# Performance work log

Measured on AMD Instinct MI355X. Metric: run time of the kernel, lower is better.

Reference implementation:

```python
import jax, jax.numpy as jnp
import numpy as np

HIDDEN = 512
BATCH = 64
SEQ = 1024
FUTURE = 16


def setup_inputs() -> dict:
    key = jax.random.key(0)
    ks = jax.random.split(key, 12)
    s = 0.05  # small init to keep the un-squashed LSTM recurrence stable
    H = HIDDEN
    inp = {
        "x": jax.random.normal(ks[0], (BATCH, SEQ), dtype=jnp.float32),
        # cell 1: input_length=1
        "W1": jax.random.normal(ks[1], (4 * H, 1), dtype=jnp.float32) * s,
        "bW1": jax.random.normal(ks[2], (4 * H,), dtype=jnp.float32) * s,
        "U1": jax.random.normal(ks[3], (4 * H, H), dtype=jnp.float32) * s,
        "bU1": jax.random.normal(ks[4], (4 * H,), dtype=jnp.float32) * s,
        # cell 2: input_length=H
        "W2": jax.random.normal(ks[5], (4 * H, H), dtype=jnp.float32) * s,
        "bW2": jax.random.normal(ks[6], (4 * H,), dtype=jnp.float32) * s,
        "U2": jax.random.normal(ks[7], (4 * H, H), dtype=jnp.float32) * s,
        "bU2": jax.random.normal(ks[8], (4 * H,), dtype=jnp.float32) * s,
        # output head: Linear(H, 1)
        "lw": jax.random.normal(ks[9], (1, H), dtype=jnp.float32) * s,
        "lb": jax.random.normal(ks[10], (1,), dtype=jnp.float32) * s,
        "future": FUTURE,
    }
    return inp


def _cell(x_t, h, c, W, bW, U, bU):
    # NOTE: faithful to source — NO sigmoid/tanh on the gates, only tanh on c_t.
    gates = x_t @ W.T + bW + h @ U.T + bU            # [B, 4H]
    i_t, f_t, g_t, o_t = jnp.split(gates, 4, axis=-1)
    c_t = f_t * c + i_t * g_t
    h_t = o_t * jnp.tanh(c_t)
    return h_t, c_t


def reference(x, W1, bW1, U1, bU1, W2, bW2, U2, bU2, lw, lb, future):
    B = x.shape[0]
    H = U1.shape[1]
    zeros = jnp.zeros((B, H), dtype=x.dtype)
    init = (zeros, zeros, zeros, zeros, jnp.zeros((B, 1), dtype=x.dtype))

    def run(carry, x_t):
        h1, c1, h2, c2, _ = carry
        h1, c1 = _cell(x_t, h1, c1, W1, bW1, U1, bU1)
        h2, c2 = _cell(h1, h2, c2, W2, bW2, U2, bU2)
        out = h2 @ lw.T + lb                          # [B, 1]
        return (h1, c1, h2, c2, out), out

    # teacher-forced pass over the observed sequence
    xs = x.T[:, :, None]                              # [T, B, 1]
    carry, outs = jax.lax.scan(run, init, xs)         # outs: [T, B, 1]

    if future > 0:
        def run_future(carry, _):
            return run(carry, carry[4])
        carry, outs_f = jax.lax.scan(run_future, carry, None, length=future)
        outs = jnp.concatenate([outs, outs_f], axis=0)

    return outs[:, :, 0].T                            # [B, T+future]
```

## Files before the change

kernel.cpp:

```cpp
#include <hip/hip_runtime.h>
#include <math.h>

#define HID 512
#define B 64
#define SEQT 1024
#define FUT 16
#define TT (SEQT + FUT)
#define NWG 256
#define TPB 512
#define TPB1 1024
#define NWAVE1 16
#define JPW 2
#define HB (HID * B)
#define BLOBF 12288

#define WS_H1_F   512
#define WS_H2_F   (WS_H1_F + 2 * HB)
#define WS_BLOB_F (WS_H2_F + 2 * HB)
#define WS_XT_F   (WS_BLOB_F + NWG * BLOBF)
#define WS_TOT_F  (WS_XT_F + SEQT * B)

__device__ inline void pub_store(float* p, float v) {
  __hip_atomic_store(p, v, __ATOMIC_RELAXED, __HIP_MEMORY_SCOPE_AGENT);
}

__device__ inline void gbar4(int* bb, int wg, int bar) {
  __builtin_amdgcn_s_waitcnt(0);
  __syncthreads();
  const int tid  = threadIdx.x;
  const int lane = tid & 63;
  if (tid == 0) {
    __hip_atomic_store(bb + wg, bar, __ATOMIC_RELAXED, __HIP_MEMORY_SCOPE_AGENT);
    __builtin_amdgcn_fence(__ATOMIC_ACQUIRE, "agent");
  }
  if (wg == NWG - 1 && tid < 64) {
    for (;;) {
      int a = __hip_atomic_load(bb + lane,       __ATOMIC_RELAXED, __HIP_MEMORY_SCOPE_AGENT);
      int b = __hip_atomic_load(bb + 64  + lane, __ATOMIC_RELAXED, __HIP_MEMORY_SCOPE_AGENT);
      int c = __hip_atomic_load(bb + 128 + lane, __ATOMIC_RELAXED, __HIP_MEMORY_SCOPE_AGENT);
      int d = __hip_atomic_load(bb + 192 + lane, __ATOMIC_RELAXED, __HIP_MEMORY_SCOPE_AGENT);
      if (__all(a >= bar && b >= bar && c >= bar && d >= bar)) break;
      __builtin_amdgcn_s_sleep(2);
    }
    if (lane == 0)
      __hip_atomic_store(bb + 320, bar, __ATOMIC_RELAXED, __HIP_MEMORY_SCOPE_AGENT);
  }
  if (tid == 0) {
    while (__hip_atomic_load(bb + 320, __ATOMIC_RELAXED,
                             __HIP_MEMORY_SCOPE_AGENT) < bar) {
      __builtin_amdgcn_s_sleep(2);
    }
  }
  __syncthreads();
}

__global__ void __launch_bounds__(256) prep_ws(
    const float* __restrict__ x,
    const float* __restrict__ U1, const float* __restrict__ W2,
    const float* __restrict__ U2, float* __restrict__ ws)
{
  const int idx = blockIdx.x * blockDim.x + threadIdx.x;
  if (idx < WS_BLOB_F) {
    ws[idx] = 0.0f;
  }
  {
    const int i2 = idx - WS_BLOB_F;
    if (i2 >= 0 && i2 < NWG * BLOBF) {
      const int wg  = i2 / BLOBF;
      const int off = i2 - wg * BLOBF;
      const int j0  = wg * JPW;
      float v;
      if (off < 4096) {
        const int k = off >> 3, r = off & 7;
        const int row = (r >> 1) * HID + j0 + (r & 1);
        v = U1[(size_t)row * HID + k];
      } else {
        const int o2 = off - 4096;
        const int k = o2 >> 4, rr = o2 & 15;
        const int r = rr & 7;
        const int row = (r >> 1) * HID + j0 + (r & 1);
        v = (rr < 8) ? W2[(size_t)row * HID + k] : U2[(size_t)row * HID + k];
      }
      ws[WS_BLOB_F + i2] = v;
    }
  }
  {
    const int i3 = idx - WS_XT_F;
    if (i3 >= 0 && i3 < SEQT * B) {
      const int t = i3 >> 6, b = i3 & 63;
      ws[WS_XT_F + i3] = x[(size_t)b * SEQT + t];
    }
  }
}

__global__ void __launch_bounds__(TPB1, 1) rnn_main(
    const float* __restrict__ W1, const float* __restrict__ bW1,
    const float* __restrict__ bU1,
    const float* __restrict__ bW2, const float* __restrict__ bU2,
    const float* __restrict__ lw, const float* __restrict__ lb,
    float* __restrict__ out,
    int* __restrict__ bb,
    float* __restrict__ h1b, float* __restrict__ h2b,
    const float* __restrict__ wbl, const float* __restrict__ xT)
{
  __shared__ float wlds[BLOBF];
  __shared__ float red[NWAVE1][8][B];
  __shared__ float outred[NWAVE1][B];
  __shared__ float c1s[JPW][B], c2s[JPW][B];
  __shared__ float w1c[8], bs1[8], bs2[8];

  const int wg   = blockIdx.x;
  const int j0   = wg * JPW;
  const int tid  = threadIdx.x;
  const int lane = tid & 63;
  const int wvu  = __builtin_amdgcn_readfirstlane(tid >> 6);

  {
    const float4* gsrc = (const float4*)(wbl + (size_t)wg * BLOBF);
    float4* ldst = (float4*)wlds;
    #pragma unroll
    for (int i = 0; i < BLOBF / 4 / TPB1; ++i)
      ldst[i * TPB1 + tid] = gsrc[i * TPB1 + tid];
  }
  if (tid < JPW * B) { c1s[tid >> 6][lane] = 0.f; c2s[tid >> 6][lane] = 0.f; }
  if (tid < 8) {
    const int g = tid >> 1, jl = tid & 1;
    const int row = g * HID + j0 + jl;
    w1c[tid] = W1[row];
    bs1[tid] = bW1[row] + bU1[row];
    bs2[tid] = bW2[row] + bU2[row];
  }
  __syncthreads();

  const float* wl1 = wlds + wvu * 256;
  const float* wl2 = wlds + 4096 + wvu * 512;
  const float lbv = lb[0];

  float4 H1[8], Q[8];
  #pragma unroll
  for (int i = 0; i < 8; ++i) H1[i] = make_float4(0.f, 0.f, 0.f, 0.f);

  int bar = 0;
  for (int t = 0; t < TT; ++t) {
    float*       h1new = h1b + (t & 1) * HB;
    const float* h2old = h2b + ((t + 1) & 1) * HB;
    float*       h2new = h2b + (t & 1) * HB;

    float xvpref = 0.f;
    if (tid < JPW * B && t < SEQT) xvpref = xT[(size_t)t * B + lane];

    {
      float a[8] = {0.f,0.f,0.f,0.f,0.f,0.f,0.f,0.f};
      #pragma unroll
      for (int c = 0; c < 8; ++c) {
        const float hh[4] = {H1[c].x, H1[c].y, H1[c].z, H1[c].w};
        #pragma unroll
        for (int j = 0; j < 4; ++j) {
          const float4 wA = *(const float4*)(wl1 + c * 32 + j * 8);
          const float4 wB = *(const float4*)(wl1 + c * 32 + j * 8 + 4);
          const float h = hh[j];
          a[0] = fmaf(wA.x, h, a[0]); a[1] = fmaf(wA.y, h, a[1]);
          a[2] = fmaf(wA.z, h, a[2]); a[3] = fmaf(wA.w, h, a[3]);
          a[4] = fmaf(wB.x, h, a[4]); a[5] = fmaf(wB.y, h, a[5]);
          a[6] = fmaf(wB.z, h, a[6]); a[7] = fmaf(wB.w, h, a[7]);
        }
      }
      #pragma unroll
      for (int r = 0; r < 8; ++r) red[wvu][r][lane] = a[r];
    }
    __syncthreads();

    if (tid < JPW * B) {
      const int jl = tid >> 6, b = tid & 63;
      const float xv = (t < SEQT) ? xvpref : out[(size_t)b * TT + (t - 1)];
      float gate[4];
      #pragma unroll
      for (int g = 0; g < 4; ++g) {
        const int r = g * 2 + jl;
        float s = bs1[r] + xv * w1c[r];
        #pragma unroll
        for (int w = 0; w < NWAVE1; ++w) s += red[w][r][b];
        gate[g] = s;
      }
      const float c = gate[1] * c1s[jl][b] + gate[0] * gate[2];
      c1s[jl][b] = c;
      const int j = j0 + jl;
      pub_store(&h1new[(size_t)(j >> 2) * (B * 4) + b * 4 + (j & 3)],
                gate[3] * tanhf(c));
    }

    ++bar;
    gbar4(bb, wg, bar);

    if (wg == (t & 127) && t >= 1 && t <= SEQT - 1) {
      const float4* hb2 = (const float4*)h2old + (size_t)(wvu * 8) * B + lane;
      const float4* lw4 = (const float4*)lw + wvu * 8;
      float p = 0.f;
      #pragma unroll
      for (int i = 0; i < 8; ++i) {
        const float4 hv = hb2[i * B];
        const float4 wv = lw4[i];
        p = fmaf(wv.x, hv.x, p); p = fmaf(wv.y, hv.y, p);
        p = fmaf(wv.z, hv.z, p); p = fmaf(wv.w, hv.w, p);
      }
      outred[wvu][lane] = p;
      __syncthreads();
      if (tid < B) {
        float o = lbv;
        #pragma unroll
        for (int s = 0; s < NWAVE1; ++s) o += outred[s][tid];
        pub_store(&out[(size_t)tid * TT + (t - 1)], o);
      }
      __syncthreads();
    }

    {
      const float4* pp4 = (const float4*)h1new + (size_t)(wvu * 8) * B + lane;
      const float4* qq4 = (const float4*)h2old + (size_t)(wvu * 8) * B + lane;
      #pragma unroll
      for (int i = 0; i < 8; ++i) H1[i] = pp4[i * B];
      #pragma unroll
      for (int i = 0; i < 8; ++i) Q[i] = qq4[i * B];
      float a[8] = {0.f,0.f,0.f,0.f,0.f,0.f,0.f,0.f};
      #pragma unroll
      for (int c = 0; c < 8; ++c) {
        const float hp_[4] = {H1[c].x, H1[c].y, H1[c].z, H1[c].w};
        const float hq_[4] = {Q[c].x, Q[c].y, Q[c].z, Q[c].w};
        #pragma unroll
        for (int j = 0; j < 4; ++j) {
          const float4 w0 = *(const float4*)(wl2 + c * 64 + j * 16);
          const float4 w1 = *(const float4*)(wl2 + c * 64 + j * 16 + 4);
          const float4 w2 = *(const float4*)(wl2 + c * 64 + j * 16 + 8);
          const float4 w3 = *(const float4*)(wl2 + c * 64 + j * 16 + 12);
          const float hp1 = hp_[j], hq1 = hq_[j];
          a[0] = fmaf(w0.x, hp1, a[0]); a[1] = fmaf(w0.y, hp1, a[1]);
          a[2] = fmaf(w0.z, hp1, a[2]); a[3] = fmaf(w0.w, hp1, a[3]);
          a[4] = fmaf(w1.x, hp1, a[4]); a[5] = fmaf(w1.y, hp1, a[5]);
          a[6] = fmaf(w1.z, hp1, a[6]); a[7] = fmaf(w1.w, hp1, a[7]);
          a[0] = fmaf(w2.x, hq1, a[0]); a[1] = fmaf(w2.y, hq1, a[1]);
          a[2] = fmaf(w2.z, hq1, a[2]); a[3] = fmaf(w2.w, hq1, a[3]);
          a[4] = fmaf(w3.x, hq1, a[4]); a[5] = fmaf(w3.y, hq1, a[5]);
          a[6] = fmaf(w3.z, hq1, a[6]); a[7] = fmaf(w3.w, hq1, a[7]);
        }
      }
      #pragma unroll
      for (int r = 0; r < 8; ++r) red[wvu][r][lane] = a[r];
    }
    __syncthreads();

    if (tid < JPW * B) {
      const int jl = tid >> 6, b = tid & 63;
      float gate[4];
      #pragma unroll
      for (int g = 0; g < 4; ++g) {
        const int r = g * 2 + jl;
        float s = bs2[r];
        #pragma unroll
        for (int w = 0; w < NWAVE1; ++w) s += red[w][r][b];
        gate[g] = s;
      }
      const float c = gate[1] * c2s[jl][b] + gate[0] * gate[2];
      c2s[jl][b] = c;
      const int j = j0 + jl;
      pub_store(&h2new[(size_t)(j >> 2) * (B * 4) + b * 4 + (j & 3)],
                gate[3] * tanhf(c));
    }
    __syncthreads();

    if (t >= SEQT - 1) {
      ++bar;
      gbar4(bb, wg, bar);
      if (wg == 0) {
        const float4* hb2 = (const float4*)h2new + (size_t)(wvu * 8) * B + lane;
        const float4* lw4 = (const float4*)lw + wvu * 8;
        float p = 0.f;
        #pragma unroll
        for (int i = 0; i < 8; ++i) {
          const float4 hv = hb2[i * B];
          const float4 wv = lw4[i];
          p = fmaf(wv.x, hv.x, p); p = fmaf(wv.y, hv.y, p);
          p = fmaf(wv.z, hv.z, p); p = fmaf(wv.w, hv.w, p);
        }
        outred[wvu][lane] = p;
        __syncthreads();
        if (tid < B) {
          float o = lbv;
          #pragma unroll
          for (int s = 0; s < NWAVE1; ++s) o += outred[s][tid];
          pub_store(&out[(size_t)tid * TT + t], o);
        }
        __syncthreads();
      }
      ++bar;
      gbar4(bb, wg, bar);
    }
  }
}

__device__ inline void gbar(int* cnt, int target) {
  __syncthreads();
  if (threadIdx.x == 0) {
    __threadfence();
    __hip_atomic_fetch_add(cnt, 1, __ATOMIC_RELEASE, __HIP_MEMORY_SCOPE_AGENT);
    while (__hip_atomic_load(cnt, __ATOMIC_ACQUIRE, __HIP_MEMORY_SCOPE_AGENT) < target) {
      __builtin_amdgcn_s_sleep(2);
    }
  }
  __syncthreads();
}

__global__ void __launch_bounds__(TPB) zero_ws(float* ws, int n) {
  int i = blockIdx.x * blockDim.x + threadIdx.x;
  if (i < n) ws[i] = 0.0f;
}

__global__ void __launch_bounds__(TPB) rnn_fallback(
    const float* __restrict__ x,
    const float* __restrict__ W1, const float* __restrict__ bW1,
    const float* __restrict__ U1, const float* __restrict__ bU1,
    const float* __restrict__ W2, const float* __restrict__ bW2,
    const float* __restrict__ U2, const float* __restrict__ bU2,
    const float* __restrict__ lw, const float* __restrict__ lb,
    float* out, float* ws)
{
  __shared__ float red[8][8][B];
  __shared__ float outred[8][B];
  __shared__ float c1s[JPW][B], c2s[JPW][B];
  __shared__ float w1c[8], bs1[8], bs2[8];

  int* cnt   = (int*)ws;
  float* h1b = ws + 16;
  float* h2b = h1b + 2 * HB;

  const int wg   = blockIdx.x;
  const int j0   = wg * JPW;
  const int tid  = threadIdx.x;
  const int lane = tid & 63;
  const int wvu  = __builtin_amdgcn_readfirstlane(tid >> 6);
  const int kb   = wvu << 6;

  if (tid < JPW * B) { c1s[tid >> 6][lane] = 0.f; c2s[tid >> 6][lane] = 0.f; }
  if (tid < 8) {
    const int g = tid >> 1, jl = tid & 1;
    const int row = g * HID + j0 + jl;
    w1c[tid] = W1[row];
    bs1[tid] = bW1[row] + bU1[row];
    bs2[tid] = bW2[row] + bU2[row];
  }
  __syncthreads();

  const float* u1p[8]; const float* w2p[8]; const float* u2p[8];
  #pragma unroll
  for (int r = 0; r < 8; ++r) {
    const int row = (r >> 1) * HID + j0 + (r & 1);
    u1p[r] = U1 + (size_t)row * HID + kb;
    w2p[r] = W2 + (size_t)row * HID + kb;
    u2p[r] = U2 + (size_t)row * HID + kb;
  }
  const float lbv = lb[0];

  int bar = 0;
  for (int t = 0; t < TT; ++t) {
    const float* h1old = h1b + ((t + 1) & 1) * HB;
    float*       h1new = h1b + (t & 1) * HB;
    const float* h2old = h2b + ((t + 1) & 1) * HB;
    float*       h2new = h2b + (t & 1) * HB;

    {
      const float* hp = h1old + (size_t)kb * B;
      float a0=0.f,a1=0.f,a2=0.f,a3=0.f,a4=0.f,a5=0.f,a6=0.f,a7=0.f;
      #pragma unroll 8
      for (int k = 0; k < 64; ++k) {
        const float hv = hp[k * B + lane];
        a0 = fmaf(u1p[0][k], hv, a0); a1 = fmaf(u1p[1][k], hv, a1);
        a2 = fmaf(u1p[2][k], hv, a2); a3 = fmaf(u1p[3][k], hv, a3);
        a4 = fmaf(u1p[4][k], hv, a4); a5 = fmaf(u1p[5][k], hv, a5);
        a6 = fmaf(u1p[6][k], hv, a6); a7 = fmaf(u1p[7][k], hv, a7);
      }
      red[wvu][0][lane]=a0; red[wvu][1][lane]=a1; red[wvu][2][lane]=a2; red[wvu][3][lane]=a3;
      red[wvu][4][lane]=a4; red[wvu][5][lane]=a5; red[wvu][6][lane]=a6; red[wvu][7][lane]=a7;
    }
    __syncthreads();

    if (tid < JPW * B) {
      const int jl = tid >> 6, b = tid & 63;
      const float xv = (t < SEQT) ? x[(size_t)b * SEQT + t]
                                  : out[(size_t)b * TT + (t - 1)];
      float gate[4];
      #pragma unroll
      for (int g = 0; g < 4; ++g) {
        const int r = g * 2 + jl;
        float s = bs1[r] + xv * w1c[r];
        #pragma unroll
        for (int w = 0; w < 8; ++w) s += red[w][r][b];
        gate[g] = s;
      }
      const float c = gate[1] * c1s[jl][b] + gate[0] * gate[2];
      c1s[jl][b] = c;
      h1new[(size_t)(j0 + jl) * B + b] = gate[3] * tanhf(c);
    }

    ++bar;
    gbar(cnt, NWG * bar);

    if (wg == 0 && t >= 1 && t <= SEQT - 1) {
      const float* hb2 = h2old + (size_t)(wvu * 64) * B;
      const float* lwp = lw + wvu * 64;
      float p = 0.f;
      #pragma unroll 8
      for (int j = 0; j < 64; ++j) p = fmaf(lwp[j], hb2[j * B + lane], p);
      outred[wvu][lane] = p;
      __syncthreads();
      if (tid < B) {
        float o = lbv;
        #pragma unroll
        for (int s = 0; s < 8; ++s) o += outred[s][tid];
        out[(size_t)tid * TT + (t - 1)] = o;
      }
      __syncthreads();
    }

    {
      const float* h1p = h1new + (size_t)kb * B;
      const float* h2p = h2old + (size_t)kb * B;
      float s0=0.f,s1=0.f,s2=0.f,s3=0.f,s4=0.f,s5=0.f,s6=0.f,s7=0.f;
      float q0=0.f,q1=0.f,q2=0.f,q3=0.f,q4=0.f,q5=0.f,q6=0.f,q7=0.f;
      #pragma unroll 4
      for (int k = 0; k < 64; ++k) {
        const float h1v = h1p[k * B + lane];
        const float h2v = h2p[k * B + lane];
        s0 = fmaf(w2p[0][k], h1v, s0); q0 = fmaf(u2p[0][k], h2v, q0);
        s1 = fmaf(w2p[1][k], h1v, s1); q1 = fmaf(u2p[1][k], h2v, q1);
        s2 = fmaf(w2p[2][k], h1v, s2); q2 = fmaf(u2p[2][k], h2v, q2);
        s3 = fmaf(w2p[3][k], h1v, s3); q3 = fmaf(u2p[3][k], h2v, q3);
        s4 = fmaf(w2p[4][k], h1v, s4); q4 = fmaf(u2p[4][k], h2v, q4);
        s5 = fmaf(w2p[5][k], h1v, s5); q5 = fmaf(u2p[5][k], h2v, q5);
        s6 = fmaf(w2p[6][k], h1v, s6); q6 = fmaf(u2p[6][k], h2v, q6);
        s7 = fmaf(w2p[7][k], h1v, s7); q7 = fmaf(u2p[7][k], h2v, q7);
      }
      red[wvu][0][lane]=s0+q0; red[wvu][1][lane]=s1+q1;
      red[wvu][2][lane]=s2+q2; red[wvu][3][lane]=s3+q3;
      red[wvu][4][lane]=s4+q4; red[wvu][5][lane]=s5+q5;
      red[wvu][6][lane]=s6+q6; red[wvu][7][lane]=s7+q7;
    }
    __syncthreads();

    if (tid < JPW * B) {
      const int jl = tid >> 6, b = tid & 63;
      float gate[4];
      #pragma unroll
      for (int g = 0; g < 4; ++g) {
        const int r = g * 2 + jl;
        float s = bs2[r];
        #pragma unroll
        for (int w = 0; w < 8; ++w) s += red[w][r][b];
        gate[g] = s;
      }
      const float c = gate[1] * c2s[jl][b] + gate[0] * gate[2];
      c2s[jl][b] = c;
      h2new[(size_t)(j0 + jl) * B + b] = gate[3] * tanhf(c);
    }
    __syncthreads();

    if (t >= SEQT - 1) {
      ++bar;
      gbar(cnt, NWG * bar);
      if (wg == 0) {
        const float* hb2 = h2new + (size_t)(wvu * 64) * B;
        const float* lwp = lw + wvu * 64;
        float p = 0.f;
        #pragma unroll 8
        for (int j = 0; j < 64; ++j) p = fmaf(lwp[j], hb2[j * B + lane], p);
        outred[wvu][lane] = p;
        __syncthreads();
        if (tid < B) {
          float o = lbv;
          #pragma unroll
          for (int s = 0; s < 8; ++s) o += outred[s][tid];
          out[(size_t)tid * TT + t] = o;
        }
        __syncthreads();
      }
      ++bar;
      gbar(cnt, NWG * bar);
    }
  }
}

extern "C" void kernel_launch(void* const* d_in, const int* in_sizes, int n_in,
                              void* d_out, int out_size, void* d_ws, size_t ws_size,
                              hipStream_t stream) {
  (void)in_sizes; (void)n_in; (void)out_size;
  const float* x   = (const float*)d_in[0];
  const float* W1  = (const float*)d_in[1];
  const float* bW1 = (const float*)d_in[2];
  const float* U1  = (const float*)d_in[3];
  const float* bU1 = (const float*)d_in[4];
  const float* W2  = (const float*)d_in[5];
  const float* bW2 = (const float*)d_in[6];
  const float* U2  = (const float*)d_in[7];
  const float* bU2 = (const float*)d_in[8];
  const float* lw  = (const float*)d_in[9];
  const float* lb  = (const float*)d_in[10];

  float* out = (float*)d_out;
  float* ws  = (float*)d_ws;

  if (ws_size >= (size_t)WS_TOT_F * sizeof(float)) {
    prep_ws<<<(WS_TOT_F + 255) / 256, 256, 0, stream>>>(x, U1, W2, U2, ws);
    rnn_main<<<NWG, TPB1, 0, stream>>>(W1, bW1, bU1, bW2, bU2, lw, lb, out,
                                       (int*)ws, ws + WS_H1_F, ws + WS_H2_F,
                                       ws + WS_BLOB_F, ws + WS_XT_F);
  } else {
    const int nzero = 16 + 4 * HID * B;
    zero_ws<<<(nzero + TPB - 1) / TPB, TPB, 0, stream>>>(ws, nzero);
    rnn_fallback<<<NWG, TPB, 0, stream>>>(x, W1, bW1, U1, bU1,
                                          W2, bW2, U2, bU2, lw, lb, out, ws);
  }
}
```

Baseline: 12.34 ms.

## Use all-to-all polling barrier and defer teacher-forced output head to the end

The grid barrier drops the single-aggregator two-hop scheme: every workgroup now polls all 256 flags directly, with a shorter sleep. During the teacher-forced phase, each workgroup writes its partial lw·h2 contribution to a workspace buffer instead of one rotating workgroup computing the output head each step. A final pass reduces the partials into the outputs. This takes the head computation off the per-step critical path and cuts barrier latency. The costs are more polling traffic on the flags and a larger workspace that must be available for the deferred path to run.

After: 11.81 ms. 4.2% less time.

```diff
diff --git a/kernel.cpp b/kernel.cpp
--- a/kernel.cpp
+++ b/kernel.cpp
@@ -19,36 +19,29 @@
 #define WS_BLOB_F (WS_H2_F + 2 * HB)
 #define WS_XT_F   (WS_BLOB_F + NWG * BLOBF)
 #define WS_TOT_F  (WS_XT_F + SEQT * B)
+#define WS_PART_F WS_TOT_F
+#define WS_TOT2_F (WS_PART_F + (size_t)SEQT * NWG * B)
 
 __device__ inline void pub_store(float* p, float v) {
   __hip_atomic_store(p, v, __ATOMIC_RELAXED, __HIP_MEMORY_SCOPE_AGENT);
 }
 
-__device__ inline void gbar4(int* bb, int wg, int bar) {
+__device__ inline void gbar5(int* bb, int wg, int bar) {
   __builtin_amdgcn_s_waitcnt(0);
   __syncthreads();
-  const int tid  = threadIdx.x;
-  const int lane = tid & 63;
+  const int tid = threadIdx.x;
   if (tid == 0) {
     __hip_atomic_store(bb + wg, bar, __ATOMIC_RELAXED, __HIP_MEMORY_SCOPE_AGENT);
     __builtin_amdgcn_fence(__ATOMIC_ACQUIRE, "agent");
   }
-  if (wg == NWG - 1 && tid < 64) {
+  if (tid < 64) {
     for (;;) {
-      int a = __hip_atomic_load(bb + lane,       __ATOMIC_RELAXED, __HIP_MEMORY_SCOPE_AGENT);
-      int b = __hip_atomic_load(bb + 64  + lane, __ATOMIC_RELAXED, __HIP_MEMORY_SCOPE_AGENT);
-      int c = __hip_atomic_load(bb + 128 + lane, __ATOMIC_RELAXED, __HIP_MEMORY_SCOPE_AGENT);
-      int d = __hip_atomic_load(bb + 192 + lane, __ATOMIC_RELAXED, __HIP_MEMORY_SCOPE_AGENT);
+      int a = __hip_atomic_load(bb + tid,       __ATOMIC_RELAXED, __HIP_MEMORY_SCOPE_AGENT);
+      int b = __hip_atomic_load(bb + 64  + tid, __ATOMIC_RELAXED, __HIP_MEMORY_SCOPE_AGENT);
+      int c = __hip_atomic_load(bb + 128 + tid, __ATOMIC_RELAXED, __HIP_MEMORY_SCOPE_AGENT);
+      int d = __hip_atomic_load(bb + 192 + tid, __ATOMIC_RELAXED, __HIP_MEMORY_SCOPE_AGENT);
       if (__all(a >= bar && b >= bar && c >= bar && d >= bar)) break;
-      __builtin_amdgcn_s_sleep(2);
-    }
-    if (lane == 0)
-      __hip_atomic_store(bb + 320, bar, __ATOMIC_RELAXED, __HIP_MEMORY_SCOPE_AGENT);
-  }
-  if (tid == 0) {
-    while (__hip_atomic_load(bb + 320, __ATOMIC_RELAXED,
-                             __HIP_MEMORY_SCOPE_AGENT) < bar) {
-      __builtin_amdgcn_s_sleep(2);
+      __builtin_amdgcn_s_sleep(1);
     }
   }
   __syncthreads();
@@ -101,13 +94,15 @@
     float* __restrict__ out,
     int* __restrict__ bb,
     float* __restrict__ h1b, float* __restrict__ h2b,
-    const float* __restrict__ wbl, const float* __restrict__ xT)
+    const float* __restrict__ wbl, const float* __restrict__ xT,
+    float* __restrict__ part, int defer)
 {
   __shared__ float wlds[BLOBF];
   __shared__ float red[NWAVE1][8][B];
   __shared__ float outred[NWAVE1][B];
   __shared__ float c1s[JPW][B], c2s[JPW][B];
-  __shared__ float w1c[8], bs1[8], bs2[8];
+  __shared__ float pout[JPW][B];
+  __shared__ float w1c[8], bs1[8], bs2[8], lwc[JPW];
 
   const int wg   = blockIdx.x;
   const int j0   = wg * JPW;
@@ -130,6 +125,7 @@
     bs1[tid] = bW1[row] + bU1[row];
     bs2[tid] = bW2[row] + bU2[row];
   }
+  if (tid < JPW) lwc[tid] = lw[j0 + tid];
   __syncthreads();
 
   const float* wl1 = wlds + wvu * 256;
@@ -190,9 +186,9 @@
     }
 
     ++bar;
-    gbar4(bb, wg, bar);
-
-    if (wg == (t & 127) && t >= 1 && t <= SEQT - 1) {
+    gbar5(bb, wg, bar);
+
+    if (!defer && wg == (t & 127) && t >= 1 && t <= SEQT - 1) {
       const float4* hb2 = (const float4*)h2old + (size_t)(wvu * 8) * B + lane;
       const float4* lw4 = (const float4*)lw + wvu * 8;
       float p = 0.f;
@@ -261,15 +257,21 @@
       }
       const float c = gate[1] * c2s[jl][b] + gate[0] * gate[2];
       c2s[jl][b] = c;
+      const float h2v = gate[3] * tanhf(c);
       const int j = j0 + jl;
-      pub_store(&h2new[(size_t)(j >> 2) * (B * 4) + b * 4 + (j & 3)],
-                gate[3] * tanhf(c));
+      pub_store(&h2new[(size_t)(j >> 2) * (B * 4) + b * 4 + (j & 3)], h2v);
+      if (defer && t < SEQT) pout[jl][b] = lwc[jl] * h2v;
     }
     __syncthreads();
+
+    if (defer && t < SEQT && tid < B) {
+      pub_store(&part[((size_t)t * NWG + wg) * B + tid],
+                pout[0][tid] + pout[1][tid]);
+    }
 
     if (t >= SEQT - 1) {
       ++bar;
-      gbar4(bb, wg, bar);
+      gbar5(bb, wg, bar);
       if (wg == 0) {
         const float4* hb2 = (const float4*)h2new + (size_t)(wvu * 8) * B + lane;
         const float4* lw4 = (const float4*)lw + wvu * 8;
@@ -292,7 +294,27 @@
         __syncthreads();
       }
       ++bar;
-      gbar4(bb, wg, bar);
+      gbar5(bb, wg, bar);
+    }
+  }
+
+  if (defer) {
+    ++bar;
+    gbar5(bb, wg, bar);
+    for (int tt = wg; tt < SEQT - 1; tt += NWG) {
+      const float* pp = part + ((size_t)tt * NWG + wvu * 16) * B + lane;
+      float s = 0.f;
+      #pragma unroll
+      for (int i = 0; i < 16; ++i) s += pp[i * B];
+      outred[wvu][lane] = s;
+      __syncthreads();
+      if (tid < B) {
+        float o = lbv;
+        #pragma unroll
+        for (int v = 0; v < NWAVE1; ++v) o += outred[v][tid];
+        out[(size_t)tid * TT + tt] = o;
+      }
+      __syncthreads();
     }
   }
 }
@@ -507,10 +529,12 @@
   float* ws  = (float*)d_ws;
 
   if (ws_size >= (size_t)WS_TOT_F * sizeof(float)) {
+    const int defer = (ws_size >= WS_TOT2_F * sizeof(float)) ? 1 : 0;
     prep_ws<<<(WS_TOT_F + 255) / 256, 256, 0, stream>>>(x, U1, W2, U2, ws);
     rnn_main<<<NWG, TPB1, 0, stream>>>(W1, bW1, bU1, bW2, bU2, lw, lb, out,
                                        (int*)ws, ws + WS_H1_F, ws + WS_H2_F,
-                                       ws + WS_BLOB_F, ws + WS_XT_F);
+                                       ws + WS_BLOB_F, ws + WS_XT_F,
+                                       ws + WS_PART_F, defer);
   } else {
     const int nzero = 16 + 4 * HID * B;
     zero_ws<<<(nzero + TPB - 1) / TPB, TPB, 0, stream>>>(ws, nzero);
```
